# Performance work log

Hardware: AMD Instinct MI355X
Metric: run time of the kernel (lower is better)

The kernel has to match this reference:

```python
import jax, jax.numpy as jnp
import numpy as np

F_DIM = 256
N_HEADS = 4
D_Q = F_DIM // N_HEADS  # 64
EPS = 1e-6


def layer_norm(x, g, b):
    mu = jnp.mean(x, axis=-1, keepdims=True)
    var = jnp.mean(jnp.square(x - mu), axis=-1, keepdims=True)
    return (x - mu) * jax.lax.rsqrt(var + EPS) * g + b


def linear(x, W, b):
    # torch nn.Linear: y = x @ W.T + b, W: [out, in]
    return jnp.einsum('...i,oi->...o', x, W) + b


def setup_inputs() -> dict:
    key = jax.random.key(0)
    ks = jax.random.split(key, 16)
    f = F_DIM
    inp = {
        'code_map': jax.random.normal(ks[0], (8, 512, f), jnp.float32),
        'texture_map': jax.random.normal(ks[1], (8, 512, f), jnp.float32),
        'Wq': jax.random.normal(ks[2], (N_HEADS * D_Q, f), jnp.float32) * 0.02,
        'bq': jnp.zeros((N_HEADS * D_Q,), jnp.float32),
        'Wk': jax.random.normal(ks[3], (N_HEADS * D_Q, f), jnp.float32) * 0.02,
        'bk': jnp.zeros((N_HEADS * D_Q,), jnp.float32),
        'Wv': jax.random.normal(ks[4], (N_HEADS * D_Q, f), jnp.float32) * 0.02,
        'bv': jnp.zeros((N_HEADS * D_Q,), jnp.float32),
        'Wo': jax.random.normal(ks[5], (f, N_HEADS * D_Q), jnp.float32) * 0.02,
        'bo': jnp.zeros((f,), jnp.float32),
        'ln1_g': jnp.ones((f,), jnp.float32), 'ln1_b': jnp.zeros((f,), jnp.float32),
        'ln2_g': jnp.ones((f,), jnp.float32), 'ln2_b': jnp.zeros((f,), jnp.float32),
        'ffln_g': jnp.ones((f,), jnp.float32), 'ffln_b': jnp.zeros((f,), jnp.float32),
        'W1': jax.random.normal(ks[6], (f, f), jnp.float32) * 0.02,
        'b1': jnp.zeros((f,), jnp.float32),
        'W2': jax.random.normal(ks[7], (f, f), jnp.float32) * 0.02,
        'b2': jnp.zeros((f,), jnp.float32),
    }
    return inp


def reference(code_map, texture_map, Wq, bq, Wk, bk, Wv, bv, Wo, bo,
              ln1_g, ln1_b, ln2_g, ln2_b, ffln_g, ffln_b, W1, b1, W2, b2):
    n_code, V, f = code_map.shape
    bs = texture_map.shape[0]
    h, dq = N_HEADS, D_Q

    # LayerNorms (code side -> ln1, texture side -> ln2); expansion via repeat
    # is a pure broadcast, so keep code side [n_code,...] and texture side [bs,...].
    code2 = layer_norm(code_map, ln1_g, ln1_b)       # [n, V, f]
    tex2 = layer_norm(texture_map, ln2_g, ln2_b)     # [b, V, f]

    q = linear(tex2, Wq, bq).reshape(bs, V, h, dq)    # [b, V, h, d]
    k = linear(code2, Wk, bk).reshape(n_code, V, h, dq)
    v = linear(code2, Wv, bv).reshape(n_code, V, h, dq)

    scale = 1.0 / jnp.sqrt(jnp.asarray(dq, q.dtype))
    # scores: [b, n, h, Vq, Vk]
    scores = jnp.einsum('bqhd,nkhd->bnhqk', q, k) * scale
    attn = jax.nn.softmax(scores, axis=-1)
    ctx = jnp.einsum('bnhqk,nkhd->bnhqd', attn, v)    # [b, n, h, V, d]
    ctx = ctx.transpose(0, 1, 3, 2, 4).reshape(bs, n_code, V, h * dq)
    feat = linear(ctx, Wo, bo)                        # [b, n, V, f]

    x = texture_map[:, None, :, :] + feat             # residual with broadcast
    # ffR: MLP_res_block
    y = layer_norm(x, ffln_g, ffln_b)
    y = linear(jax.nn.relu(linear(y, W1, b1)), W2, b2)
    return x + y
```

## Files before the change

kernel.cpp:

```cpp
#include <hip/hip_runtime.h>
#include <hip/hip_bf16.h>

#define F 256
#define V 512
#define NB 8
#define NC 8
#define NH 4
#define DQ 64
#define EPS 1e-6f

typedef __hip_bfloat16 bf16;
typedef __attribute__((ext_vector_type(8))) short short8;
typedef __attribute__((ext_vector_type(4))) float f32x4;
typedef __attribute__((ext_vector_type(4))) unsigned uint4v;

__device__ __forceinline__ float b2f(bf16 x){ return __bfloat162float(x); }
__device__ __forceinline__ float shf(short s){
    return __bfloat162float(__builtin_bit_cast(bf16, (unsigned short)s));
}

#define MFMA(a,b,c) __builtin_amdgcn_mfma_f32_16x16x32_bf16((a),(b),(c),0,0,0)

__device__ __forceinline__ unsigned pack2bf(float a, float b){
    unsigned short ua = __builtin_bit_cast(unsigned short, __float2bfloat16(a));
    unsigned short ub = __builtin_bit_cast(unsigned short, __float2bfloat16(b));
    return (unsigned)ua | ((unsigned)ub << 16);
}

__global__ __launch_bounds__(256) void pre_kernel(const float* __restrict__ code,
                          const float* __restrict__ tex,
                          const float* __restrict__ ln1_g, const float* __restrict__ ln1_b,
                          const float* __restrict__ ln2_g, const float* __restrict__ ln2_b,
                          const float* __restrict__ w0, const float* __restrict__ w1,
                          const float* __restrict__ w2, const float* __restrict__ w3,
                          const float* __restrict__ w4, const float* __restrict__ w5,
                          bf16* __restrict__ cn, bf16* __restrict__ tn, bf16* __restrict__ tb,
                          bf16* __restrict__ wdst){
    if (blockIdx.x >= 2048){
        int bid = blockIdx.x - 2048;
        int which = bid >> 6;
        int idx = (((bid & 63) << 8) | threadIdx.x) << 2;
        const float* s = which==0?w0: which==1?w1: which==2?w2: which==3?w3: which==4?w4: w5;
        float4 v = *(const float4*)(s + idx);
        uint2 p; p.x = pack2bf(v.x, v.y); p.y = pack2bf(v.z, v.w);
        *(uint2*)(wdst + which * (F*F) + idx) = p;
        return;
    }
    int w = threadIdx.x >> 6, lane = threadIdx.x & 63;
    int r = blockIdx.x * 4 + w;
    int is_tex = r >> 12;
    int row = r & 4095;
    const float* src = is_tex ? tex : code;
    const float* g   = is_tex ? ln2_g : ln1_g;
    const float* be  = is_tex ? ln2_b : ln1_b;
    bf16* dst        = is_tex ? tn : cn;

    float4 x = *(const float4*)(src + row * F + lane * 4);
    if (is_tex){
        uint2 p; p.x = pack2bf(x.x, x.y); p.y = pack2bf(x.z, x.w);
        *(uint2*)(tb + row * F + lane * 4) = p;
    }
    float s = x.x + x.y + x.z + x.w;
    #pragma unroll
    for(int m = 1; m < 64; m <<= 1) s += __shfl_xor(s, m);
    float mu = s * (1.0f / F);
    float d0 = x.x - mu, d1 = x.y - mu, d2 = x.z - mu, d3 = x.w - mu;
    float q = d0*d0 + d1*d1 + d2*d2 + d3*d3;
    #pragma unroll
    for(int m = 1; m < 64; m <<= 1) q += __shfl_xor(q, m);
    float rs = rsqrtf(q * (1.0f / F) + EPS);
    float4 gg = *(const float4*)(g + lane * 4);
    float4 bb = *(const float4*)(be + lane * 4);
    uint2 p;
    p.x = pack2bf(d0 * rs * gg.x + bb.x, d1 * rs * gg.y + bb.y);
    p.y = pack2bf(d2 * rs * gg.z + bb.z, d3 * rs * gg.w + bb.w);
    *(uint2*)(dst + row * F + lane * 4) = p;
}

__global__ __launch_bounds__(256)
void qkv_kernel(const bf16* __restrict__ cn,
                const bf16* __restrict__ tn,
                const bf16* __restrict__ wbf,
                const float* __restrict__ bq,
                const float* __restrict__ bk,
                const float* __restrict__ bv,
                bf16* __restrict__ qn,
                bf16* __restrict__ k4,
                bf16* __restrict__ v4){
    __shared__ bf16 ts[64][72];
    int which = blockIdx.z;
    const bf16* in   = (which == 0) ? tn : cn;
    const bf16* wb   = wbf + which * (F * F);
    const float* bias = (which == 0) ? bq : (which == 1) ? bk : bv;

    int tid = threadIdx.x;
    int w = tid >> 6, lane = tid & 63;
    int lg = lane >> 4, li = lane & 15;
    int rowbase = blockIdx.x * 64 + w * 16;
    int colbase = blockIdx.y * 64;

    f32x4 acc[4];
    #pragma unroll
    for(int ni = 0; ni < 4; ni++) acc[ni] = (f32x4){0.f,0.f,0.f,0.f};

    const bf16* arow = in + (rowbase + li) * F + lg * 8;
    const bf16* brow = wb + (colbase + li) * F + lg * 8;

    #pragma unroll
    for(int kc = 0; kc < 8; kc++){
        short8 a = *(const short8*)(arow + kc * 32);
        #pragma unroll
        for(int ni = 0; ni < 4; ni++){
            short8 bbf = *(const short8*)(brow + ni * 16 * F + kc * 32);
            acc[ni] = MFMA(a, bbf, acc[ni]);
        }
    }

    if (which < 2){
        #pragma unroll
        for(int ni = 0; ni < 4; ni++)
            #pragma unroll
            for(int r = 0; r < 4; r++)
                ts[w * 16 + lg * 4 + r][ni * 16 + li] =
                    __float2bfloat16(acc[ni][r] + bias[colbase + ni * 16 + li]);
    } else {
        #pragma unroll
        for(int ni = 0; ni < 4; ni++)
            #pragma unroll
            for(int r = 0; r < 4; r++)
                ts[ni * 16 + li][w * 16 + lg * 4 + r] =
                    __float2bfloat16(acc[ni][r] + bias[colbase + ni * 16 + li]);
    }
    __syncthreads();

    if (which == 0){
        int rr = tid >> 2, gg2 = tid & 3;
        *(short8*)(qn + (blockIdx.x * 64 + rr) * F + colbase + gg2 * 16)
            = *(const short8*)&ts[rr][gg2 * 16];
    } else if (which == 1){
        int n = blockIdx.x >> 3;
        int kc2base = (blockIdx.x & 7) * 2;
        int hh = blockIdx.y;
        #pragma unroll
        for(int rep = 0; rep < 2; rep++){
            int c = tid + 256 * rep;
            int f = c >> 6, wf = c & 63;
            int lgp = wf >> 4, lip = wf & 15;
            int kc2l = f >> 2, kt = (f >> 1) & 1, ks = f & 1;
            int keysel = ((lip >> 2) * 8) + kt * 4 + (lip & 3);
            int fi = ((n * 16 + kc2base + kc2l) * 2 + kt) * 8 + hh * 2 + ks;
            *(short8*)(k4 + fi * 512 + lgp * 128 + lip * 8)
                = *(const short8*)&ts[kc2l * 32 + keysel][ks * 32 + lgp * 8];
        }
    } else {
        int col = tid & 63, half = tid >> 6;
        int keybase = blockIdx.x * 64;
        int n = keybase >> 9;
        int keyl = (keybase & (V - 1)) + half * 16;
        int chunk = keyl >> 5, off = keyl & 31;
        *(short8*)(v4 + ((n * 16 + chunk) * F + colbase + col) * 32 + off)
            = *(const short8*)&ts[col][half * 16];
    }
}

__global__ __launch_bounds__(512) void attn_mlp_kernel(const bf16* __restrict__ qn,
                                                       const bf16* __restrict__ k4,
                                                       const bf16* __restrict__ v4,
                                                       const bf16* __restrict__ wbf,
                                                       const float* __restrict__ bo,
                                                       const bf16* __restrict__ tb,
                                                       const float* __restrict__ ffg,
                                                       const float* __restrict__ ffb,
                                                       const float* __restrict__ b1,
                                                       const float* __restrict__ b2,
                                                       float* __restrict__ out){
    __shared__ bf16 xs[64][264];
    int n = blockIdx.x & 7, b = blockIdx.x >> 3, qt = blockIdx.y;
    int tid = threadIdx.x;
    int w = tid >> 6, lane = tid & 63;
    int h = w & 3, qh = w >> 2;
    int lg = lane >> 4, li = lane & 15;

    short8 qB[2][2];
    #pragma unroll
    for(int qq = 0; qq < 2; qq++)
        #pragma unroll
        for(int ks = 0; ks < 2; ks++)
            qB[qq][ks] = *(const short8*)(qn + (b * V + qt * 64 + qh * 32 + qq * 16 + li) * F
                                             + h * DQ + ks * 32 + lg * 8);

    f32x4 o[2][4];
    #pragma unroll
    for(int qq = 0; qq < 2; qq++)
        #pragma unroll
        for(int dt = 0; dt < 4; dt++) o[qq][dt] = (f32x4){0.f,0.f,0.f,0.f};
    float l_acc[2] = {0.f, 0.f};

    const float cexp = 0.125f * 1.44269504088896f;
    int fel = lg * 128 + li * 8;

    #pragma unroll
    for(int kc = 0; kc < 16; kc++){
        int fb = ((n * 16 + kc) * 2) * 8 + h * 2;
        short8 kA0 = *(const short8*)(k4 + (fb + 0) * 512 + fel);
        short8 kA1 = *(const short8*)(k4 + (fb + 1) * 512 + fel);
        short8 kA2 = *(const short8*)(k4 + (fb + 8) * 512 + fel);
        short8 kA3 = *(const short8*)(k4 + (fb + 9) * 512 + fel);
        const bf16* vb = v4 + ((n * 16 + kc) * F + h * DQ) * 32;
        short8 vA0 = *(const short8*)(vb + (0 * 16 + li) * 32 + lg * 8);
        short8 vA1 = *(const short8*)(vb + (1 * 16 + li) * 32 + lg * 8);
        short8 vA2 = *(const short8*)(vb + (2 * 16 + li) * 32 + lg * 8);
        short8 vA3 = *(const short8*)(vb + (3 * 16 + li) * 32 + lg * 8);

        #pragma unroll
        for(int qq = 0; qq < 2; qq++){
            f32x4 st0 = (f32x4){0.f,0.f,0.f,0.f};
            f32x4 st1 = (f32x4){0.f,0.f,0.f,0.f};
            __builtin_amdgcn_s_setprio(1);
            st0 = MFMA(kA0, qB[qq][0], st0);
            st1 = MFMA(kA2, qB[qq][0], st1);
            st0 = MFMA(kA1, qB[qq][1], st0);
            st1 = MFMA(kA3, qB[qq][1], st1);
            __builtin_amdgcn_s_setprio(0);

            float p0[4], p1[4], rsum = 0.f;
            #pragma unroll
            for(int r = 0; r < 4; r++){
                p0[r] = exp2f(st0[r] * cexp);
                p1[r] = exp2f(st1[r] * cexp);
                rsum += p0[r] + p1[r];
            }
            l_acc[qq] += rsum;

            uint4v uv;
            uv.x = pack2bf(p0[0], p0[1]);
            uv.y = pack2bf(p0[2], p0[3]);
            uv.z = pack2bf(p1[0], p1[1]);
            uv.w = pack2bf(p1[2], p1[3]);
            short8 pfrag = __builtin_bit_cast(short8, uv);

            __builtin_amdgcn_s_setprio(1);
            o[qq][0] = MFMA(vA0, pfrag, o[qq][0]);
            o[qq][1] = MFMA(vA1, pfrag, o[qq][1]);
            o[qq][2] = MFMA(vA2, pfrag, o[qq][2]);
            o[qq][3] = MFMA(vA3, pfrag, o[qq][3]);
            __builtin_amdgcn_s_setprio(0);
        }
    }

    float inv[2];
    #pragma unroll
    for(int qq = 0; qq < 2; qq++){
        l_acc[qq] += __shfl_xor(l_acc[qq], 16);
        l_acc[qq] += __shfl_xor(l_acc[qq], 32);
        inv[qq] = 1.0f / l_acc[qq];
    }

    #pragma unroll
    for(int qq = 0; qq < 2; qq++)
        #pragma unroll
        for(int dt = 0; dt < 4; dt++){
            uint2 pkd;
            pkd.x = pack2bf(o[qq][dt][0] * inv[qq], o[qq][dt][1] * inv[qq]);
            pkd.y = pack2bf(o[qq][dt][2] * inv[qq], o[qq][dt][3] * inv[qq]);
            *(uint2*)&xs[qh * 32 + qq * 16 + li][h * DQ + dt * 16 + lg * 4] = pkd;
        }
    __syncthreads();

    const bf16* Wo = wbf + 3 * (F * F);
    int colbase = w * 32;
    f32x4 xac[4][2];
    #pragma unroll
    for(int mi = 0; mi < 4; mi++)
        #pragma unroll
        for(int ni = 0; ni < 2; ni++) xac[mi][ni] = (f32x4){0.f,0.f,0.f,0.f};
    #pragma unroll
    for(int kc = 0; kc < 8; kc++){
        short8 a[4];
        #pragma unroll
        for(int mi = 0; mi < 4; mi++)
            a[mi] = *(const short8*)&xs[mi * 16 + li][kc * 32 + lg * 8];
        #pragma unroll
        for(int ni = 0; ni < 2; ni++){
            short8 bw = *(const short8*)(Wo + (colbase + ni * 16 + li) * F + kc * 32 + lg * 8);
            #pragma unroll
            for(int mi = 0; mi < 4; mi++)
                xac[mi][ni] = MFMA(a[mi], bw, xac[mi][ni]);
        }
    }
    float xres[4][2][4];
    #pragma unroll
    for(int mi = 0; mi < 4; mi++)
        #pragma unroll
        for(int r = 0; r < 4; r++){
            int qrel = mi * 16 + lg * 4 + r;
            #pragma unroll
            for(int ni = 0; ni < 2; ni++){
                int col = colbase + ni * 16 + li;
                xres[mi][ni][r] = xac[mi][ni][r] + bo[col]
                                + b2f(tb[(b * V + qt * 64 + qrel) * F + col]);
            }
        }
    __syncthreads();
    #pragma unroll
    for(int mi = 0; mi < 4; mi++)
        #pragma unroll
        for(int r = 0; r < 4; r++){
            int qrel = mi * 16 + lg * 4 + r;
            #pragma unroll
            for(int ni = 0; ni < 2; ni++)
                xs[qrel][colbase + ni * 16 + li] = __float2bfloat16(xres[mi][ni][r]);
        }
    __syncthreads();

    int row = tid >> 3, sub = tid & 7;
    short8 xv[4];
    #pragma unroll
    for(int seg = 0; seg < 4; seg++)
        xv[seg] = *(const short8*)&xs[row][sub * 32 + seg * 8];
    float sum = 0.f, sq = 0.f;
    #pragma unroll
    for(int seg = 0; seg < 4; seg++)
        #pragma unroll
        for(int j = 0; j < 8; j++){
            float v0 = shf(xv[seg][j]);
            sum += v0; sq += v0 * v0;
        }
    #pragma unroll
    for(int m = 1; m < 8; m <<= 1){
        sum += __shfl_xor(sum, m);
        sq  += __shfl_xor(sq, m);
    }
    float mu = sum * (1.0f / F);
    float var = sq * (1.0f / F) - mu * mu;
    float rsv = rsqrtf(var + EPS);
    #pragma unroll
    for(int seg = 0; seg < 4; seg++){
        int c = sub * 32 + seg * 8;
        float4 g0 = *(const float4*)(ffg + c);
        float4 g1 = *(const float4*)(ffg + c + 4);
        float4 f0 = *(const float4*)(ffb + c);
        float4 f1 = *(const float4*)(ffb + c + 4);
        float n0 = (shf(xv[seg][0]) - mu) * rsv * g0.x + f0.x;
        float n1 = (shf(xv[seg][1]) - mu) * rsv * g0.y + f0.y;
        float n2 = (shf(xv[seg][2]) - mu) * rsv * g0.z + f0.z;
        float n3 = (shf(xv[seg][3]) - mu) * rsv * g0.w + f0.w;
        float n4 = (shf(xv[seg][4]) - mu) * rsv * g1.x + f1.x;
        float n5 = (shf(xv[seg][5]) - mu) * rsv * g1.y + f1.y;
        float n6 = (shf(xv[seg][6]) - mu) * rsv * g1.z + f1.z;
        float n7 = (shf(xv[seg][7]) - mu) * rsv * g1.w + f1.w;
        uint4v pk;
        pk.x = pack2bf(n0, n1); pk.y = pack2bf(n2, n3);
        pk.z = pack2bf(n4, n5); pk.w = pack2bf(n6, n7);
        *(short8*)&xs[row][c] = __builtin_bit_cast(short8, pk);
    }
    __syncthreads();

    const bf16* W1b = wbf + 4 * (F * F);
    f32x4 hac[4][2];
    #pragma unroll
    for(int mi = 0; mi < 4; mi++)
        #pragma unroll
        for(int ni = 0; ni < 2; ni++) hac[mi][ni] = (f32x4){0.f,0.f,0.f,0.f};
    #pragma unroll
    for(int kc = 0; kc < 8; kc++){
        short8 a[4];
        #pragma unroll
        for(int mi = 0; mi < 4; mi++)
            a[mi] = *(const short8*)&xs[mi * 16 + li][kc * 32 + lg * 8];
        #pragma unroll
        for(int ni = 0; ni < 2; ni++){
            short8 bw = *(const short8*)(W1b + (colbase + ni * 16 + li) * F + kc * 32 + lg * 8);
            #pragma unroll
            for(int mi = 0; mi < 4; mi++)
                hac[mi][ni] = MFMA(a[mi], bw, hac[mi][ni]);
        }
    }
    __syncthreads();
    #pragma unroll
    for(int mi = 0; mi < 4; mi++)
        #pragma unroll
        for(int r = 0; r < 4; r++){
            int rr = mi * 16 + lg * 4 + r;
            #pragma unroll
            for(int ni = 0; ni < 2; ni++){
                int col = colbase + ni * 16 + li;
                xs[rr][col] = __float2bfloat16(fmaxf(hac[mi][ni][r] + b1[col], 0.f));
            }
        }
    __syncthreads();

    const bf16* W2b = wbf + 5 * (F * F);
    f32x4 oac[4][2];
    #pragma unroll
    for(int mi = 0; mi < 4; mi++)
        #pragma unroll
        for(int ni = 0; ni < 2; ni++) oac[mi][ni] = (f32x4){0.f,0.f,0.f,0.f};
    #pragma unroll
    for(int kc = 0; kc < 8; kc++){
        short8 a[4];
        #pragma unroll
        for(int mi = 0; mi < 4; mi++)
            a[mi] = *(const short8*)&xs[mi * 16 + li][kc * 32 + lg * 8];
        #pragma unroll
        for(int ni = 0; ni < 2; ni++){
            short8 bw = *(const short8*)(W2b + (colbase + ni * 16 + li) * F + kc * 32 + lg * 8);
            #pragma unroll
            for(int mi = 0; mi < 4; mi++)
                oac[mi][ni] = MFMA(a[mi], bw, oac[mi][ni]);
        }
    }
    #pragma unroll
    for(int mi = 0; mi < 4; mi++)
        #pragma unroll
        for(int r = 0; r < 4; r++){
            int qrel = mi * 16 + lg * 4 + r;
            int ro = (b * NC + n) * V + qt * 64 + qrel;
            #pragma unroll
            for(int ni = 0; ni < 2; ni++){
                int col = colbase + ni * 16 + li;
                out[ro * F + col] = oac[mi][ni][r] + b2[col] + xres[mi][ni][r];
            }
        }
}

extern "C" void kernel_launch(void* const* d_in, const int* in_sizes, int n_in,
                              void* d_out, int out_size, void* d_ws, size_t ws_size,
                              hipStream_t stream) {
    const float* code_map = (const float*)d_in[0];
    const float* tex_map  = (const float*)d_in[1];
    const float* Wq = (const float*)d_in[2];  const float* bq = (const float*)d_in[3];
    const float* Wk = (const float*)d_in[4];  const float* bk = (const float*)d_in[5];
    const float* Wv = (const float*)d_in[6];  const float* bv = (const float*)d_in[7];
    const float* Wo = (const float*)d_in[8];  const float* bo = (const float*)d_in[9];
    const float* ln1_g = (const float*)d_in[10]; const float* ln1_b = (const float*)d_in[11];
    const float* ln2_g = (const float*)d_in[12]; const float* ln2_b = (const float*)d_in[13];
    const float* ffln_g = (const float*)d_in[14]; const float* ffln_b = (const float*)d_in[15];
    const float* W1 = (const float*)d_in[16]; const float* b1 = (const float*)d_in[17];
    const float* W2 = (const float*)d_in[18]; const float* b2 = (const float*)d_in[19];
    float* out = (float*)d_out;

    bf16* ws  = (bf16*)d_ws;
    bf16* qn  = ws;
    bf16* k4  = qn + 1048576;
    bf16* v4  = k4 + 1048576;
    bf16* cn  = v4 + 1048576;
    bf16* tn  = cn + 1048576;
    bf16* tb  = tn + 1048576;
    bf16* wbf = tb + 1048576;

    pre_kernel<<<2048 + 384, 256, 0, stream>>>(code_map, tex_map, ln1_g, ln1_b, ln2_g, ln2_b,
                                               Wq, Wk, Wv, Wo, W1, W2, cn, tn, tb, wbf);
    qkv_kernel<<<dim3(64, 4, 3), 256, 0, stream>>>(cn, tn, wbf, bq, bk, bv, qn, k4, v4);
    attn_mlp_kernel<<<dim3(64, 8), 512, 0, stream>>>(qn, k4, v4, wbf, bo, tb,
                                                     ffln_g, ffln_b, b1, b2, out);
}
```

Before: 192.8 us.

## Fuse LayerNorm and weight conversion into QKV kernel, fold softmax scale, MFMA row-sum

```diff
diff --git a/kernel.cpp b/kernel.cpp
--- a/kernel.cpp
+++ b/kernel.cpp
@@ -8,6 +8,7 @@
 #define NH 4
 #define DQ 64
 #define EPS 1e-6f
+#define CEXPQ 0.18033688f
 
 typedef __hip_bfloat16 bf16;
 typedef __attribute__((ext_vector_type(8))) short short8;
@@ -27,102 +28,107 @@
     return (unsigned)ua | ((unsigned)ub << 16);
 }
 
-__global__ __launch_bounds__(256) void pre_kernel(const float* __restrict__ code,
-                          const float* __restrict__ tex,
-                          const float* __restrict__ ln1_g, const float* __restrict__ ln1_b,
-                          const float* __restrict__ ln2_g, const float* __restrict__ ln2_b,
-                          const float* __restrict__ w0, const float* __restrict__ w1,
-                          const float* __restrict__ w2, const float* __restrict__ w3,
-                          const float* __restrict__ w4, const float* __restrict__ w5,
-                          bf16* __restrict__ cn, bf16* __restrict__ tn, bf16* __restrict__ tb,
-                          bf16* __restrict__ wdst){
-    if (blockIdx.x >= 2048){
-        int bid = blockIdx.x - 2048;
-        int which = bid >> 6;
-        int idx = (((bid & 63) << 8) | threadIdx.x) << 2;
-        const float* s = which==0?w0: which==1?w1: which==2?w2: which==3?w3: which==4?w4: w5;
-        float4 v = *(const float4*)(s + idx);
+__global__ __launch_bounds__(256)
+void qkv_kernel(const float* __restrict__ code, const float* __restrict__ tex,
+                const float* __restrict__ wq_f, const float* __restrict__ wk_f,
+                const float* __restrict__ wv_f, const float* __restrict__ wo_f,
+                const float* __restrict__ w1_f, const float* __restrict__ w2_f,
+                const float* __restrict__ ln1_g, const float* __restrict__ ln1_b,
+                const float* __restrict__ ln2_g, const float* __restrict__ ln2_b,
+                const float* __restrict__ bq, const float* __restrict__ bk,
+                const float* __restrict__ bv,
+                bf16* __restrict__ qn, bf16* __restrict__ k4, bf16* __restrict__ v4,
+                bf16* __restrict__ tb, bf16* __restrict__ wbf){
+    int tid = threadIdx.x;
+    if (blockIdx.x >= 64){
+        int flat = (blockIdx.z * 16 + (blockIdx.x - 64)) * 4 + blockIdx.y;
+        int idx = flat * 1024 + tid * 4;
+        int which = idx >> 16;
+        const float* s = which == 0 ? wo_f : which == 1 ? w1_f : w2_f;
+        int local = idx & 65535;
+        float4 v = *(const float4*)(s + local);
         uint2 p; p.x = pack2bf(v.x, v.y); p.y = pack2bf(v.z, v.w);
-        *(uint2*)(wdst + which * (F*F) + idx) = p;
+        *(uint2*)(wbf + (3 + which) * (F * F) + local) = p;
         return;
     }
-    int w = threadIdx.x >> 6, lane = threadIdx.x & 63;
-    int r = blockIdx.x * 4 + w;
-    int is_tex = r >> 12;
-    int row = r & 4095;
-    const float* src = is_tex ? tex : code;
-    const float* g   = is_tex ? ln2_g : ln1_g;
-    const float* be  = is_tex ? ln2_b : ln1_b;
-    bf16* dst        = is_tex ? tn : cn;
-
-    float4 x = *(const float4*)(src + row * F + lane * 4);
-    if (is_tex){
-        uint2 p; p.x = pack2bf(x.x, x.y); p.y = pack2bf(x.z, x.w);
-        *(uint2*)(tb + row * F + lane * 4) = p;
-    }
-    float s = x.x + x.y + x.z + x.w;
-    #pragma unroll
-    for(int m = 1; m < 64; m <<= 1) s += __shfl_xor(s, m);
-    float mu = s * (1.0f / F);
-    float d0 = x.x - mu, d1 = x.y - mu, d2 = x.z - mu, d3 = x.w - mu;
-    float q = d0*d0 + d1*d1 + d2*d2 + d3*d3;
-    #pragma unroll
-    for(int m = 1; m < 64; m <<= 1) q += __shfl_xor(q, m);
-    float rs = rsqrtf(q * (1.0f / F) + EPS);
-    float4 gg = *(const float4*)(g + lane * 4);
-    float4 bb = *(const float4*)(be + lane * 4);
-    uint2 p;
-    p.x = pack2bf(d0 * rs * gg.x + bb.x, d1 * rs * gg.y + bb.y);
-    p.y = pack2bf(d2 * rs * gg.z + bb.z, d3 * rs * gg.w + bb.w);
-    *(uint2*)(dst + row * F + lane * 4) = p;
-}
-
-__global__ __launch_bounds__(256)
-void qkv_kernel(const bf16* __restrict__ cn,
-                const bf16* __restrict__ tn,
-                const bf16* __restrict__ wbf,
-                const float* __restrict__ bq,
-                const float* __restrict__ bk,
-                const float* __restrict__ bv,
-                bf16* __restrict__ qn,
-                bf16* __restrict__ k4,
-                bf16* __restrict__ v4){
+
+    __shared__ bf16 lnb[64][264];
     __shared__ bf16 ts[64][72];
     int which = blockIdx.z;
-    const bf16* in   = (which == 0) ? tn : cn;
-    const bf16* wb   = wbf + which * (F * F);
+    const float* src  = (which == 0) ? tex : code;
+    const float* g    = (which == 0) ? ln2_g : ln1_g;
+    const float* be   = (which == 0) ? ln2_b : ln1_b;
+    const float* wsrc = (which == 0) ? wq_f : (which == 1) ? wk_f : wv_f;
     const float* bias = (which == 0) ? bq : (which == 1) ? bk : bv;
 
-    int tid = threadIdx.x;
     int w = tid >> 6, lane = tid & 63;
     int lg = lane >> 4, li = lane & 15;
     int rowbase = blockIdx.x * 64 + w * 16;
     int colbase = blockIdx.y * 64;
 
+    float4 gg = *(const float4*)(g + lane * 4);
+    float4 bb = *(const float4*)(be + lane * 4);
+    bool wtb = (which == 0) && (blockIdx.y == 0);
+
+    #pragma unroll
+    for(int half = 0; half < 2; half++){
+        float4 xr[8];
+        #pragma unroll
+        for(int r8 = 0; r8 < 8; r8++)
+            xr[r8] = *(const float4*)(src + (rowbase + half * 8 + r8) * F + lane * 4);
+        #pragma unroll
+        for(int r8 = 0; r8 < 8; r8++){
+            int row = rowbase + half * 8 + r8;
+            float4 x = xr[r8];
+            if (wtb){
+                uint2 p; p.x = pack2bf(x.x, x.y); p.y = pack2bf(x.z, x.w);
+                *(uint2*)(tb + row * F + lane * 4) = p;
+            }
+            float s = x.x + x.y + x.z + x.w;
+            float q = x.x * x.x + x.y * x.y + x.z * x.z + x.w * x.w;
+            #pragma unroll
+            for(int m = 1; m < 64; m <<= 1){
+                s += __shfl_xor(s, m);
+                q += __shfl_xor(q, m);
+            }
+            float mu = s * (1.0f / F);
+            float var = q * (1.0f / F) - mu * mu;
+            float rs = rsqrtf(var + EPS);
+            uint2 p;
+            p.x = pack2bf((x.x - mu) * rs * gg.x + bb.x, (x.y - mu) * rs * gg.y + bb.y);
+            p.y = pack2bf((x.z - mu) * rs * gg.z + bb.z, (x.w - mu) * rs * gg.w + bb.w);
+            *(uint2*)&lnb[w * 16 + half * 8 + r8][lane * 4] = p;
+        }
+    }
+
     f32x4 acc[4];
     #pragma unroll
     for(int ni = 0; ni < 4; ni++) acc[ni] = (f32x4){0.f,0.f,0.f,0.f};
 
-    const bf16* arow = in + (rowbase + li) * F + lg * 8;
-    const bf16* brow = wb + (colbase + li) * F + lg * 8;
-
     #pragma unroll
     for(int kc = 0; kc < 8; kc++){
-        short8 a = *(const short8*)(arow + kc * 32);
+        short8 a = *(const short8*)&lnb[w * 16 + li][kc * 32 + lg * 8];
         #pragma unroll
         for(int ni = 0; ni < 4; ni++){
-            short8 bbf = *(const short8*)(brow + ni * 16 * F + kc * 32);
+            const float* wp = wsrc + (colbase + ni * 16 + li) * F + kc * 32 + lg * 8;
+            float4 b0 = *(const float4*)(wp);
+            float4 b1 = *(const float4*)(wp + 4);
+            uint4v ub;
+            ub.x = pack2bf(b0.x, b0.y); ub.y = pack2bf(b0.z, b0.w);
+            ub.z = pack2bf(b1.x, b1.y); ub.w = pack2bf(b1.z, b1.w);
+            short8 bbf = __builtin_bit_cast(short8, ub);
             acc[ni] = MFMA(a, bbf, acc[ni]);
         }
     }
 
+    float cscale = (which == 0) ? CEXPQ : 1.0f;
     if (which < 2){
         #pragma unroll
         for(int ni = 0; ni < 4; ni++)
             #pragma unroll
             for(int r = 0; r < 4; r++)
                 ts[w * 16 + lg * 4 + r][ni * 16 + li] =
-                    __float2bfloat16(acc[ni][r] + bias[colbase + ni * 16 + li]);
+                    __float2bfloat16((acc[ni][r] + bias[colbase + ni * 16 + li]) * cscale);
     } else {
         #pragma unroll
         for(int ni = 0; ni < 4; ni++)
@@ -189,14 +195,18 @@
             qB[qq][ks] = *(const short8*)(qn + (b * V + qt * 64 + qh * 32 + qq * 16 + li) * F
                                              + h * DQ + ks * 32 + lg * 8);
 
-    f32x4 o[2][4];
-    #pragma unroll
-    for(int qq = 0; qq < 2; qq++)
+    f32x4 o[2][4], ls[2];
+    #pragma unroll
+    for(int qq = 0; qq < 2; qq++){
         #pragma unroll
         for(int dt = 0; dt < 4; dt++) o[qq][dt] = (f32x4){0.f,0.f,0.f,0.f};
-    float l_acc[2] = {0.f, 0.f};
-
-    const float cexp = 0.125f * 1.44269504088896f;
+        ls[qq] = (f32x4){0.f,0.f,0.f,0.f};
+    }
+
+    short8 ones8;
+    #pragma unroll
+    for(int j = 0; j < 8; j++) ones8[j] = (short)0x3F80;
+
     int fel = lg * 128 + li * 8;
 
     #pragma unroll
@@ -223,14 +233,12 @@
             st1 = MFMA(kA3, qB[qq][1], st1);
             __builtin_amdgcn_s_setprio(0);
 
-            float p0[4], p1[4], rsum = 0.f;
+            float p0[4], p1[4];
             #pragma unroll
             for(int r = 0; r < 4; r++){
-                p0[r] = exp2f(st0[r] * cexp);
-                p1[r] = exp2f(st1[r] * cexp);
-                rsum += p0[r] + p1[r];
-            }
-            l_acc[qq] += rsum;
+                p0[r] = exp2f(st0[r]);
+                p1[r] = exp2f(st1[r]);
+            }
 
             uint4v uv;
             uv.x = pack2bf(p0[0], p0[1]);
@@ -244,17 +252,14 @@
             o[qq][1] = MFMA(vA1, pfrag, o[qq][1]);
             o[qq][2] = MFMA(vA2, pfrag, o[qq][2]);
             o[qq][3] = MFMA(vA3, pfrag, o[qq][3]);
+            ls[qq] = MFMA(ones8, pfrag, ls[qq]);
             __builtin_amdgcn_s_setprio(0);
         }
     }
 
     float inv[2];
     #pragma unroll
-    for(int qq = 0; qq < 2; qq++){
-        l_acc[qq] += __shfl_xor(l_acc[qq], 16);
-        l_acc[qq] += __shfl_xor(l_acc[qq], 32);
-        inv[qq] = 1.0f / l_acc[qq];
-    }
+    for(int qq = 0; qq < 2; qq++) inv[qq] = 1.0f / ls[qq][0];
 
     #pragma unroll
     for(int qq = 0; qq < 2; qq++)
@@ -444,14 +449,13 @@
     bf16* qn  = ws;
     bf16* k4  = qn + 1048576;
     bf16* v4  = k4 + 1048576;
-    bf16* cn  = v4 + 1048576;
-    bf16* tn  = cn + 1048576;
-    bf16* tb  = tn + 1048576;
+    bf16* tb  = v4 + 1048576;
     bf16* wbf = tb + 1048576;
 
-    pre_kernel<<<2048 + 384, 256, 0, stream>>>(code_map, tex_map, ln1_g, ln1_b, ln2_g, ln2_b,
-                                               Wq, Wk, Wv, Wo, W1, W2, cn, tn, tb, wbf);
-    qkv_kernel<<<dim3(64, 4, 3), 256, 0, stream>>>(cn, tn, wbf, bq, bk, bv, qn, k4, v4);
+    qkv_kernel<<<dim3(80, 4, 3), 256, 0, stream>>>(code_map, tex_map,
+                                                   Wq, Wk, Wv, Wo, W1, W2,
+                                                   ln1_g, ln1_b, ln2_g, ln2_b,
+                                                   bq, bk, bv, qn, k4, v4, tb, wbf);
     attn_mlp_kernel<<<dim3(64, 8), 512, 0, stream>>>(qn, k4, v4, wbf, bo, tb,
                                                      ffln_g, ffln_b, b1, b2, out);
 }
```

Result: no change. 193.4 us (+0.3%).
